# Optimization experiments

Measured on AMD Instinct MI355X. Metric: run time of the kernel, lower is better.

## Reference

```python
import jax, jax.numpy as jnp
import numpy as np

B, LOOKBACK, N_STOCKS, D_MODEL, D_K, D_V, MAX_LAG = 64, 32, 256, 512, 128, 128, 16


def setup_inputs() -> dict:
    key = jax.random.key(0)
    ks = jax.random.split(key, 7)
    return {
        "query_stock_emb": jax.random.normal(ks[0], (B, D_MODEL), dtype=jnp.float32),
        "all_stock_embs": jax.random.normal(ks[1], (B, LOOKBACK, N_STOCKS, D_MODEL), dtype=jnp.float32),
        "W_q": jax.random.normal(ks[2], (D_K, D_MODEL), dtype=jnp.float32) * 0.02,
        "W_k": jax.random.normal(ks[3], (D_K, D_MODEL), dtype=jnp.float32) * 0.02,
        "W_v": jax.random.normal(ks[4], (D_V, D_MODEL), dtype=jnp.float32) * 0.02,
        "lags": jax.random.uniform(ks[5], (N_STOCKS,), dtype=jnp.float32) * MAX_LAG,
        "causal_gates": jax.random.normal(ks[6], (N_STOCKS,), dtype=jnp.float32) * 0.1,
        "max_lag": MAX_LAG,
    }


def reference(query_stock_emb, all_stock_embs, W_q, W_k, W_v, lags, causal_gates, max_lag):
    lookback = all_stock_embs.shape[1]
    n_stocks = all_stock_embs.shape[2]
    d_k = W_q.shape[0]

    q = query_stock_emb @ W_q.T                        # (B, d_k)
    gates = jax.nn.sigmoid(causal_gates)               # (S,)
    lag = jax.nn.sigmoid(lags) * max_lag               # (S,)

    lag_floor = jnp.clip(jnp.floor(lag), 0, lookback - 1).astype(jnp.int32)
    lag_ceil = jnp.clip(jnp.ceil(lag), 0, lookback - 1).astype(jnp.int32)
    alpha = lag - lag_floor.astype(lag.dtype)          # (S,)

    s_idx = jnp.arange(n_stocks)
    emb_floor = all_stock_embs[:, lag_floor, s_idx, :]  # (B, S, D)
    emb_ceil = all_stock_embs[:, lag_ceil, s_idx, :]    # (B, S, D)
    a = alpha[None, :, None]
    stock_emb = (1.0 - a) * emb_floor + a * emb_ceil    # (B, S, D)

    k = jnp.einsum("bsd,kd->bsk", stock_emb, W_k)       # (B, S, d_k)
    v = jnp.einsum("bsd,vd->bsv", stock_emb, W_v)       # (B, S, d_v)

    scores = jnp.einsum("bk,bsk->bs", q, k) / np.sqrt(d_k).astype(jnp.float32)
    scores = scores * gates[None, :]
    attn = jax.nn.softmax(scores, axis=1)               # (B, S)
    context = jnp.einsum("bs,bsv->bv", attn, v)         # (B, d_v)
    return context
```

## Files before the change

kernel.cpp:

```cpp
#include <hip/hip_runtime.h>
#include <math.h>

#define B_    64
#define LOOKB 32
#define NS    256
#define DM    512
#define DK    128
#define DV    128

__device__ __forceinline__ float sigmoidf_(float x) {
    return 1.0f / (1.0f + expf(-x));
}

__device__ __forceinline__ float load_maxlag(const void* p) {
    int vi = *(const int*)p;
    if (vi >= 0 && vi < (1 << 23)) return (float)vi;
    return *(const float*)p;
}

__device__ __forceinline__ void lag_params(const float* __restrict__ lags,
                                           float maxlag, int s,
                                           int& lf, int& lc, float& alpha) {
    float lag = sigmoidf_(lags[s]) * maxlag;
    float lf_f = fminf(fmaxf(floorf(lag), 0.0f), (float)(LOOKB - 1));
    float lc_f = fminf(fmaxf(ceilf(lag), 0.0f), (float)(LOOKB - 1));
    lf = (int)lf_f;
    lc = (int)lc_f;
    alpha = lag - lf_f;
}

__global__ void k_prep(const float* __restrict__ query,
                       const float* __restrict__ Wq,
                       const float* __restrict__ Wk,
                       float* __restrict__ ws_m) {
    __shared__ float qe[DM];
    __shared__ float qv[DK];
    const int b = blockIdx.x;
    const int tid = threadIdx.x;

    qe[tid]       = query[b * DM + tid];
    qe[tid + 256] = query[b * DM + tid + 256];
    __syncthreads();

    if (tid < DK) {
        const float4* wr = (const float4*)(Wq + (size_t)tid * DM);
        const float4* qr = (const float4*)qe;
        float acc = 0.f;
#pragma unroll 8
        for (int i = 0; i < DM / 4; ++i) {
            float4 w = wr[i], q4 = qr[i];
            acc += w.x * q4.x + w.y * q4.y + w.z * q4.z + w.w * q4.w;
        }
        qv[tid] = acc;
    }
    __syncthreads();

    for (int d = tid; d < DM; d += 256) {
        float acc = 0.f;
#pragma unroll 8
        for (int k = 0; k < DK; ++k)
            acc += qv[k] * Wk[(size_t)k * DM + d];
        ws_m[b * DM + d] = acc;
    }
}

__global__ void k_scores(const float* __restrict__ embs,
                         const float* __restrict__ lags,
                         const float* __restrict__ gates,
                         const void*  __restrict__ maxlag_p,
                         const float* __restrict__ ws_m,
                         float* __restrict__ ws_scores) {
    const int tid  = threadIdx.x;
    const int b     = blockIdx.x >> 6;
    const int sbase = (blockIdx.x & 63) << 2;
    const int wave  = tid >> 6;
    const int lane  = tid & 63;
    const int s     = sbase + wave;

    const float maxlag = load_maxlag(maxlag_p);
    int lf, lc; float alpha;
    lag_params(lags, maxlag, s, lf, lc, alpha);
    const float gate = sigmoidf_(gates[s]);

    const size_t off = (size_t)lane * 8;
    const float* mrow = ws_m + (size_t)b * DM + off;
    float4 m0 = *(const float4*)(mrow);
    float4 m1 = *(const float4*)(mrow + 4);

    const size_t bf = (((size_t)b * LOOKB + lf) * NS + s) * (size_t)DM + off;
    const size_t bc = (((size_t)b * LOOKB + lc) * NS + s) * (size_t)DM + off;
    float4 f0 = *(const float4*)(embs + bf);
    float4 f1 = *(const float4*)(embs + bf + 4);
    float4 c0 = *(const float4*)(embs + bc);
    float4 c1 = *(const float4*)(embs + bc + 4);

    float acc = m0.x * (f0.x + alpha * (c0.x - f0.x))
              + m0.y * (f0.y + alpha * (c0.y - f0.y))
              + m0.z * (f0.z + alpha * (c0.z - f0.z))
              + m0.w * (f0.w + alpha * (c0.w - f0.w))
              + m1.x * (f1.x + alpha * (c1.x - f1.x))
              + m1.y * (f1.y + alpha * (c1.y - f1.y))
              + m1.z * (f1.z + alpha * (c1.z - f1.z))
              + m1.w * (f1.w + alpha * (c1.w - f1.w));

#pragma unroll
    for (int off2 = 32; off2; off2 >>= 1)
        acc += __shfl_xor(acc, off2, 64);

    if (lane == 0)
        ws_scores[b * NS + s] = gate * acc * 0.0883883476483184405f;
}

__global__ void k_softmax(const float* __restrict__ ws_scores,
                          float* __restrict__ ws_attn) {
    __shared__ float rmax[4];
    __shared__ float rsum[4];
    const int b = blockIdx.x, tid = threadIdx.x;
    const int wave = tid >> 6, lane = tid & 63;

    float v = ws_scores[b * NS + tid];
    float m = v;
#pragma unroll
    for (int off = 32; off; off >>= 1)
        m = fmaxf(m, __shfl_xor(m, off, 64));
    if (lane == 0) rmax[wave] = m;
    __syncthreads();
    const float mx = fmaxf(fmaxf(rmax[0], rmax[1]), fmaxf(rmax[2], rmax[3]));

    float e = expf(v - mx);
    float ssum = e;
#pragma unroll
    for (int off = 32; off; off >>= 1)
        ssum += __shfl_xor(ssum, off, 64);
    if (lane == 0) rsum[wave] = ssum;
    __syncthreads();
    const float tot = rsum[0] + rsum[1] + rsum[2] + rsum[3];

    ws_attn[b * NS + tid] = e / tot;
}

__global__ void k_ctx(const float* __restrict__ embs,
                      const float* __restrict__ lags,
                      const void*  __restrict__ maxlag_p,
                      const float* __restrict__ ws_attn,
                      float* __restrict__ ws_part) {
    const int b     = blockIdx.x >> 3;
    const int chunk = blockIdx.x & 7;
    const int tid   = threadIdx.x;
    const int d0    = tid * 2;
    const float maxlag = load_maxlag(maxlag_p);

    float ax = 0.f, ay = 0.f;
    const int s0 = chunk * 32;
#pragma unroll 4
    for (int i = 0; i < 32; ++i) {
        const int s = s0 + i;
        int lf, lc; float alpha;
        lag_params(lags, maxlag, s, lf, lc, alpha);
        const float w = ws_attn[b * NS + s];

        const size_t bf = (((size_t)b * LOOKB + lf) * NS + s) * (size_t)DM + d0;
        const size_t bc = (((size_t)b * LOOKB + lc) * NS + s) * (size_t)DM + d0;
        float2 ef = *(const float2*)(embs + bf);
        float2 ec = *(const float2*)(embs + bc);
        ax += w * (ef.x + alpha * (ec.x - ef.x));
        ay += w * (ef.y + alpha * (ec.y - ef.y));
    }
    float2 outv; outv.x = ax; outv.y = ay;
    *(float2*)(ws_part + ((size_t)(b * 8 + chunk)) * DM + d0) = outv;
}

__global__ void k_out(const float* __restrict__ ws_part,
                      const float* __restrict__ Wv,
                      float* __restrict__ out) {
    __shared__ float ctx[DM];
    const int b = blockIdx.x, tid = threadIdx.x;

    for (int d = tid; d < DM; d += 128) {
        float a = 0.f;
#pragma unroll
        for (int c = 0; c < 8; ++c)
            a += ws_part[((size_t)(b * 8 + c)) * DM + d];
        ctx[d] = a;
    }
    __syncthreads();

    const float4* wr = (const float4*)(Wv + (size_t)tid * DM);
    const float4* cr = (const float4*)ctx;
    float acc = 0.f;
#pragma unroll 8
    for (int i = 0; i < DM / 4; ++i) {
        float4 w = wr[i], c = cr[i];
        acc += w.x * c.x + w.y * c.y + w.z * c.z + w.w * c.w;
    }
    out[b * DV + tid] = acc;
}

extern "C" void kernel_launch(void* const* d_in, const int* in_sizes, int n_in,
                              void* d_out, int out_size, void* d_ws, size_t ws_size,
                              hipStream_t stream) {
    const float* query = (const float*)d_in[0];
    const float* embs  = (const float*)d_in[1];
    const float* Wq    = (const float*)d_in[2];
    const float* Wk    = (const float*)d_in[3];
    const float* Wv    = (const float*)d_in[4];
    const float* lags  = (const float*)d_in[5];
    const float* gates = (const float*)d_in[6];
    const void*  maxlag_p = d_in[7];

    float* out = (float*)d_out;

    float* ws        = (float*)d_ws;
    float* ws_m      = ws;
    float* ws_scores = ws + 32768;
    float* ws_attn   = ws + 49152;
    float* ws_part   = ws + 65536;
    (void)in_sizes; (void)n_in; (void)out_size; (void)ws_size;

    k_prep<<<B_, 256, 0, stream>>>(query, Wq, Wk, ws_m);
    k_scores<<<B_ * 64, 256, 0, stream>>>(embs, lags, gates, maxlag_p, ws_m, ws_scores);
    k_softmax<<<B_, 256, 0, stream>>>(ws_scores, ws_attn);
    k_ctx<<<B_ * 8, 256, 0, stream>>>(embs, lags, maxlag_p, ws_attn, ws_part);
    k_out<<<B_, 128, 0, stream>>>(ws_part, Wv, out);
}
```

Baseline: 1.198 ms.

## Fuse softmax into context kernel and restructure gather into per-wave float4 rows

Removes the separate softmax kernel: each context block recomputes the row max and sum from the raw scores. Lag parameters and attention weights for its 32 stocks are precomputed once into shared memory. The gather loop now gives each wave 8 stocks and each lane 8 contiguous floats with float4 loads, followed by a cross-wave reduction in shared memory. This saves one launch and the attention round trip through global memory, and widens loads. The cost is redundant softmax work in every block plus extra barriers and shared-memory traffic.

```diff
diff --git a/kernel.cpp b/kernel.cpp
--- a/kernel.cpp
+++ b/kernel.cpp
@@ -111,62 +111,80 @@
         ws_scores[b * NS + s] = gate * acc * 0.0883883476483184405f;
 }
 
-__global__ void k_softmax(const float* __restrict__ ws_scores,
-                          float* __restrict__ ws_attn) {
-    __shared__ float rmax[4];
-    __shared__ float rsum[4];
-    const int b = blockIdx.x, tid = threadIdx.x;
-    const int wave = tid >> 6, lane = tid & 63;
-
-    float v = ws_scores[b * NS + tid];
-    float m = v;
-#pragma unroll
-    for (int off = 32; off; off >>= 1)
-        m = fmaxf(m, __shfl_xor(m, off, 64));
-    if (lane == 0) rmax[wave] = m;
-    __syncthreads();
-    const float mx = fmaxf(fmaxf(rmax[0], rmax[1]), fmaxf(rmax[2], rmax[3]));
-
-    float e = expf(v - mx);
-    float ssum = e;
-#pragma unroll
-    for (int off = 32; off; off >>= 1)
-        ssum += __shfl_xor(ssum, off, 64);
-    if (lane == 0) rsum[wave] = ssum;
-    __syncthreads();
-    const float tot = rsum[0] + rsum[1] + rsum[2] + rsum[3];
-
-    ws_attn[b * NS + tid] = e / tot;
-}
-
 __global__ void k_ctx(const float* __restrict__ embs,
                       const float* __restrict__ lags,
                       const void*  __restrict__ maxlag_p,
-                      const float* __restrict__ ws_attn,
+                      const float* __restrict__ ws_scores,
                       float* __restrict__ ws_part) {
+    __shared__ float rred[8];
+    __shared__ float attn_sm[32];
+    __shared__ int   lf_sm[32];
+    __shared__ int   lc_sm[32];
+    __shared__ float al_sm[32];
+    __shared__ float red[4][DM];
+
     const int b     = blockIdx.x >> 3;
     const int chunk = blockIdx.x & 7;
     const int tid   = threadIdx.x;
-    const int d0    = tid * 2;
+    const int wave  = tid >> 6;
+    const int lane  = tid & 63;
     const float maxlag = load_maxlag(maxlag_p);
-
-    float ax = 0.f, ay = 0.f;
     const int s0 = chunk * 32;
-#pragma unroll 4
-    for (int i = 0; i < 32; ++i) {
-        const int s = s0 + i;
+
+    float v = ws_scores[b * NS + tid];
+    float mx = v;
+#pragma unroll
+    for (int o = 32; o; o >>= 1) mx = fmaxf(mx, __shfl_xor(mx, o, 64));
+    if (lane == 0) rred[wave] = mx;
+    __syncthreads();
+    mx = fmaxf(fmaxf(rred[0], rred[1]), fmaxf(rred[2], rred[3]));
+    float e = expf(v - mx);
+    float sm = e;
+#pragma unroll
+    for (int o = 32; o; o >>= 1) sm += __shfl_xor(sm, o, 64);
+    if (lane == 0) rred[4 + wave] = sm;
+    __syncthreads();
+    const float tot = rred[4] + rred[5] + rred[6] + rred[7];
+
+    if (tid < 32) {
+        const int s = s0 + tid;
+        attn_sm[tid] = expf(ws_scores[b * NS + s] - mx) / tot;
         int lf, lc; float alpha;
         lag_params(lags, maxlag, s, lf, lc, alpha);
-        const float w = ws_attn[b * NS + s];
-
-        const size_t bf = (((size_t)b * LOOKB + lf) * NS + s) * (size_t)DM + d0;
-        const size_t bc = (((size_t)b * LOOKB + lc) * NS + s) * (size_t)DM + d0;
-        float2 ef = *(const float2*)(embs + bf);
-        float2 ec = *(const float2*)(embs + bc);
-        ax += w * (ef.x + alpha * (ec.x - ef.x));
-        ay += w * (ef.y + alpha * (ec.y - ef.y));
-    }
-    float2 outv; outv.x = ax; outv.y = ay;
+        lf_sm[tid] = lf; lc_sm[tid] = lc; al_sm[tid] = alpha;
+    }
+    __syncthreads();
+
+    const size_t doff = (size_t)lane * 8;
+    float4 a0 = {0.f, 0.f, 0.f, 0.f}, a1 = {0.f, 0.f, 0.f, 0.f};
+#pragma unroll
+    for (int i = 0; i < 8; ++i) {
+        const int sl = wave * 8 + i;
+        const int s  = s0 + sl;
+        const float w   = attn_sm[sl];
+        const float al  = al_sm[sl];
+        const float wf  = w * (1.0f - al);
+        const float wc  = w * al;
+        const size_t bf = (((size_t)b * LOOKB + lf_sm[sl]) * NS + s) * (size_t)DM + doff;
+        const size_t bc = (((size_t)b * LOOKB + lc_sm[sl]) * NS + s) * (size_t)DM + doff;
+        float4 f0 = *(const float4*)(embs + bf);
+        float4 f1 = *(const float4*)(embs + bf + 4);
+        float4 c0 = *(const float4*)(embs + bc);
+        float4 c1 = *(const float4*)(embs + bc + 4);
+        a0.x += wf * f0.x + wc * c0.x;  a0.y += wf * f0.y + wc * c0.y;
+        a0.z += wf * f0.z + wc * c0.z;  a0.w += wf * f0.w + wc * c0.w;
+        a1.x += wf * f1.x + wc * c1.x;  a1.y += wf * f1.y + wc * c1.y;
+        a1.z += wf * f1.z + wc * c1.z;  a1.w += wf * f1.w + wc * c1.w;
+    }
+
+    *(float4*)(&red[wave][doff])     = a0;
+    *(float4*)(&red[wave][doff + 4]) = a1;
+    __syncthreads();
+
+    const int d0 = tid * 2;
+    float sx = red[0][d0]     + red[1][d0]     + red[2][d0]     + red[3][d0];
+    float sy = red[0][d0 + 1] + red[1][d0 + 1] + red[2][d0 + 1] + red[3][d0 + 1];
+    float2 outv; outv.x = sx; outv.y = sy;
     *(float2*)(ws_part + ((size_t)(b * 8 + chunk)) * DM + d0) = outv;
 }
 
@@ -213,13 +231,11 @@
     float* ws        = (float*)d_ws;
     float* ws_m      = ws;
     float* ws_scores = ws + 32768;
-    float* ws_attn   = ws + 49152;
     float* ws_part   = ws + 65536;
     (void)in_sizes; (void)n_in; (void)out_size; (void)ws_size;
 
     k_prep<<<B_, 256, 0, stream>>>(query, Wq, Wk, ws_m);
     k_scores<<<B_ * 64, 256, 0, stream>>>(embs, lags, gates, maxlag_p, ws_m, ws_scores);
-    k_softmax<<<B_, 256, 0, stream>>>(ws_scores, ws_attn);
-    k_ctx<<<B_ * 8, 256, 0, stream>>>(embs, lags, maxlag_p, ws_attn, ws_part);
+    k_ctx<<<B_ * 8, 256, 0, stream>>>(embs, lags, maxlag_p, ws_scores, ws_part);
     k_out<<<B_, 128, 0, stream>>>(ws_part, Wv, out);
 }
```

New measurement: 1.220 ms. About the same (+1.8%).
